# Optimization experiments

Hardware: AMD Instinct MI355X
Metric: run time of the kernel (lower is better)

The kernel has to match this reference:

```python
import jax, jax.numpy as jnp
import numpy as np

N_HEAD = 16
LN_EPS = 1e-5     # torch LayerNorm default
ATTN_EPS = 1e-6   # fast-transformers CausalLinearAttention eps


def layer_norm(x, g, b):
    mu = x.mean(-1, keepdims=True)
    var = ((x - mu) ** 2).mean(-1, keepdims=True)
    return (x - mu) * jax.lax.rsqrt(var + LN_EPS) * g + b


def favor(x, omega):
    # Favor/Performer softmax-kernel features.
    # x: [B,S,H,dh], omega: [dh, m/2] -> phi: [B,S,H,m] with m = 2*(dh//2) = dh
    dh = x.shape[-1]
    m = 2 * omega.shape[-1]
    xs = x * (dh ** -0.25)  # x * sqrt(softmax_temp), softmax_temp = 1/sqrt(dh)
    u = jnp.einsum('bshd,dm->bshm', xs, omega)
    h = 0.5 * jnp.sum(xs * xs, axis=-1, keepdims=True)  # ||x||^2 / 2
    return jnp.concatenate([jnp.exp(u - h), jnp.exp(-u - h)], axis=-1) * (m ** -0.5)


def causal_linear_attention(q, k, v):
    # q,k: [B,S,H,M] feature-mapped; v: [B,S,H,Dv]
    # out[i] = (phiQ_i @ sum_{j<=i} phiK_j v_j^T) / (phiQ_i . sum_{j<=i} phiK_j)
    B, S, H, M = q.shape
    Dv = v.shape[-1]
    qT = jnp.moveaxis(q, 1, 0)  # [S,B,H,M]
    kT = jnp.moveaxis(k, 1, 0)
    vT = jnp.moveaxis(v, 1, 0)  # [S,B,H,Dv]
    S0 = jnp.zeros((B, H, M, Dv), q.dtype)
    z0 = jnp.zeros((B, H, M), q.dtype)

    def step(carry, qkv):
        Sst, zst = carry
        qi, ki, vi = qkv
        Sst = Sst + ki[..., :, None] * vi[..., None, :]  # [B,H,M,Dv]
        zst = zst + ki                                   # [B,H,M]
        num = jnp.einsum('bhm,bhmd->bhd', qi, Sst)
        den = jnp.einsum('bhm,bhm->bh', qi, zst) + ATTN_EPS
        return (Sst, zst), num / den[..., None]

    _, out = jax.lax.scan(step, (S0, z0), (qT, kT, vT))
    return jnp.moveaxis(out, 0, 1)  # [B,S,H,Dv]


def forward(x, Wq, bq, Wk, bk, Wv, bv, Wo, bo, omega,
            ln1_g, ln1_b, ln2_g, ln2_b, W1, bf1, W2, bf2):
    L = Wq.shape[0]
    B, S, D = x.shape
    dh = D // N_HEAD
    out = x
    for l in range(L):  # fixed small layer count
        q = (out @ Wq[l] + bq[l]).reshape(B, S, N_HEAD, dh)
        k = (out @ Wk[l] + bk[l]).reshape(B, S, N_HEAD, dh)
        v = (out @ Wv[l] + bv[l]).reshape(B, S, N_HEAD, dh)
        Qf = favor(q, omega[l])
        Kf = favor(k, omega[l])
        a = causal_linear_attention(Qf, Kf, v).reshape(B, S, D)
        a = a @ Wo[l] + bo[l]
        h = layer_norm(out + a, ln1_g[l], ln1_b[l])          # norm1 (post-norm)
        y = jax.nn.relu(h @ W1[l] + bf1[l]) @ W2[l] + bf2[l]  # FFN
        out = layer_norm(h + y, ln2_g[l], ln2_b[l])          # norm2
    return out


def setup_inputs() -> dict:
    key = jax.random.key(0)
    L, B, S, D, DFF = 3, 2, 1024, 1024, 4096
    dh = D // N_HEAD
    ks = jax.random.split(key, 8)
    g = lambda k, shape: jax.random.normal(k, shape, jnp.float32) * 0.02
    return {
        'x': jax.random.normal(ks[0], (B, S, D), jnp.float32),
        'Wq': g(ks[1], (L, D, D)), 'bq': jnp.zeros((L, D), jnp.float32),
        'Wk': g(ks[2], (L, D, D)), 'bk': jnp.zeros((L, D), jnp.float32),
        'Wv': g(ks[3], (L, D, D)), 'bv': jnp.zeros((L, D), jnp.float32),
        'Wo': g(ks[4], (L, D, D)), 'bo': jnp.zeros((L, D), jnp.float32),
        'omega': jax.random.normal(ks[5], (L, dh, dh // 2), jnp.float32),
        'ln1_g': jnp.ones((L, D), jnp.float32), 'ln1_b': jnp.zeros((L, D), jnp.float32),
        'ln2_g': jnp.ones((L, D), jnp.float32), 'ln2_b': jnp.zeros((L, D), jnp.float32),
        'W1': g(ks[6], (L, D, DFF)), 'bf1': jnp.zeros((L, DFF), jnp.float32),
        'W2': g(ks[7], (L, DFF, D)), 'bf2': jnp.zeros((L, D), jnp.float32),
    }


def reference(x, Wq, bq, Wk, bk, Wv, bv, Wo, bo, omega,
              ln1_g, ln1_b, ln2_g, ln2_b, W1, bf1, W2, bf2):
    return forward(x, Wq, bq, Wk, bk, Wv, bv, Wo, bo, omega,
                   ln1_g, ln1_b, ln2_g, ln2_b, W1, bf1, W2, bf2)
```

## Files before the change

### kernel.cpp

```cpp
#include <hip/hip_runtime.h>

typedef unsigned int u32;
typedef unsigned short u16;
typedef unsigned long long u64;

#define LN_EPS 1e-5f
#define ATTN_EPS 1e-6f

typedef __bf16 bf16x8 __attribute__((ext_vector_type(8)));
typedef short shortx8 __attribute__((ext_vector_type(8)));
typedef float fx4 __attribute__((ext_vector_type(4)));
typedef float fx16 __attribute__((ext_vector_type(16)));

__device__ __forceinline__ u16 f2bf(float f){
  union{float f; u32 u;} x; x.f = f;
  u32 r = 0x7fffu + ((x.u>>16)&1u);
  return (u16)((x.u + r)>>16);
}
__device__ __forceinline__ float bf2f(u16 u){
  union{u32 u; float f;} x; x.u = ((u32)u)<<16; return x.f;
}
__device__ __forceinline__ bf16x8 ldfrag(const u16* p){
  return __builtin_bit_cast(bf16x8, *(const shortx8*)p);
}

__device__ __forceinline__ void async16(const void* g, void* l){
  typedef const __attribute__((address_space(1))) void gas_t;
  typedef __attribute__((address_space(3))) void las_t;
  __builtin_amdgcn_global_load_lds((gas_t*)(u64)g, (las_t*)(u32)(u64)l, 16, 0, 0);
}

__global__ void detect_kernel(const u16* __restrict__ ln1g, int* __restrict__ flag){
  if (threadIdx.x == 0 && blockIdx.x == 0)
    *flag = (ln1g[0] == 0x3F80u) ? 1 : 0;
}

__global__ __launch_bounds__(256) void cvt_small(
    const void* p0, const void* p1, const void* p2, const void* p3,
    const void* p4, const void* p5, const void* p6, const void* p7,
    const void* p8, const void* p9, const void* p10,
    float* __restrict__ out, const int* __restrict__ flagp)
{
  int i = blockIdx.x*256 + threadIdx.x;
  if (i >= 46080) return;
  const void* src; int off;
  if      (i < 3072)  { src=p0;  off=i; }
  else if (i < 6144)  { src=p1;  off=i-3072; }
  else if (i < 9216)  { src=p2;  off=i-6144; }
  else if (i < 12288) { src=p3;  off=i-9216; }
  else if (i < 18432) { src=p4;  off=i-12288; }
  else if (i < 21504) { src=p5;  off=i-18432; }
  else if (i < 24576) { src=p6;  off=i-21504; }
  else if (i < 27648) { src=p7;  off=i-24576; }
  else if (i < 30720) { src=p8;  off=i-27648; }
  else if (i < 43008) { src=p9;  off=i-30720; }
  else                { src=p10; off=i-43008; }
  float v;
  if (*flagp){ union{u32 u; float f;} x; x.u = ((u32)((const u16*)src)[off])<<16; v = x.f; }
  else v = ((const float*)src)[off];
  out[i] = v;
}

__global__ __launch_bounds__(256) void cvt_x(const void* __restrict__ in, float* __restrict__ out,
                                             u16* __restrict__ outbf, int n, const int* __restrict__ flagp){
  int i = blockIdx.x*256 + threadIdx.x;
  if (i >= n) return;
  float v;
  if (*flagp){ union{u32 u; float f;} x; x.u = ((u32)((const u16*)in)[i])<<16; v = x.f; }
  else v = ((const float*)in)[i];
  out[i] = v;
  outbf[i] = f2bf(v);
}

__global__ __launch_bounds__(256) void transpose_cvtL(
    const void* __restrict__ W, u16* __restrict__ Wt,
    int K, int N, size_t zsrc, size_t zdst, const int* __restrict__ flagp)
{
  __shared__ float s[32][33];
  const size_t eoff = (size_t)blockIdx.z * zsrc;
  Wt += (size_t)blockIdx.z * zdst;
  const int bx = blockIdx.x, by = blockIdx.y;
  const int tid = threadIdx.x;
  const int c = tid & 31, r = tid >> 5;
  const int isbf = *flagp;
#pragma unroll
  for (int i = 0; i < 4; ++i){
    int k = by*32 + r + i*8, n = bx*32 + c;
    size_t idx = eoff + (size_t)k*N + n;
    float v;
    if (isbf){ union{u32 u; float f;} x; x.u = ((u32)((const u16*)W)[idx])<<16; v = x.f; }
    else v = ((const float*)W)[idx];
    s[r + i*8][c] = v;
  }
  __syncthreads();
#pragma unroll
  for (int i = 0; i < 4; ++i){
    int n = bx*32 + r + i*8, k = by*32 + c;
    Wt[(size_t)n*K + k] = f2bf(s[c][r + i*8]);
  }
}

__global__ __launch_bounds__(256) void transpose_cvtQ(
    const void* __restrict__ W0, const void* __restrict__ W1,
    const void* __restrict__ W2, const void* __restrict__ W3,
    u16* __restrict__ Wt, const int* __restrict__ flagp)
{
  __shared__ float s[32][33];
  const int z = blockIdx.z, l = z >> 2, m = z & 3;
  const void* W = (m==0)?W0:((m==1)?W1:((m==2)?W2:W3));
  const size_t eoff = (size_t)l * 1048576;
  Wt += (size_t)z * 1048576;
  const int bx = blockIdx.x, by = blockIdx.y;
  const int tid = threadIdx.x;
  const int c = tid & 31, r = tid >> 5;
  const int isbf = *flagp;
#pragma unroll
  for (int i = 0; i < 4; ++i){
    int k = by*32 + r + i*8, n = bx*32 + c;
    size_t idx = eoff + (size_t)k*1024 + n;
    float v;
    if (isbf){ union{u32 u; float f;} x; x.u = ((u32)((const u16*)W)[idx])<<16; v = x.f; }
    else v = ((const float*)W)[idx];
    s[r + i*8][c] = v;
  }
  __syncthreads();
#pragma unroll
  for (int i = 0; i < 4; ++i){
    int n = bx*32 + r + i*8, k = by*32 + c;
    Wt[(size_t)n*1024 + k] = f2bf(s[c][r + i*8]);
  }
}

__global__ __launch_bounds__(512, 2) void mfma_gemm8(
    const u16* __restrict__ A, const u16* __restrict__ W,
    const float* __restrict__ bias,
    float* __restrict__ C, u16* __restrict__ Cbf,
    int N, int Kst, int kstep_z, int klen,
    size_t wz, size_t cz, int bz, int bias_all, int relu)
{
  __shared__ u16 As[3][256*64];
  __shared__ u16 Bs[3][128*64];
  const int z = blockIdx.z;
  W    += (size_t)z * wz;
  bias += (size_t)z * bz;
  if (C) C += (size_t)z * cz;
  const int kbeg = z * kstep_z;
  const int tid = threadIdx.x;
  const int lane = tid & 63, wid = tid >> 6;
  const size_t KstS = (size_t)Kst;

  int bx = blockIdx.x, by = blockIdx.y;
  {
    const int gx = gridDim.x, gy = gridDim.y;
    if (((gx & 3) == 0) && ((gy & 1) == 0)) {
      const int cw = gx >> 2, ch = gy >> 1;
      if (((cw & (cw-1)) == 0) && ((ch & (ch-1)) == 0)) {
        const int o = by*gx + bx;
        const int xcd = o & 7, k = o >> 3;
        const int lgw = 31 - __clz(cw);
        bx = (xcd & 3)*cw + (k & (cw-1));
        by = (xcd >> 2)*ch + (k >> lgw);
      }
    }
  }
  const int row0 = by * 256, col0 = bx * 128;

  const int sR = tid >> 3;
  const int sC = ((tid & 7) ^ (sR & 7)) << 3;
  const u16* gAr = A + (size_t)(row0 + sR)*KstS + kbeg + sC;
  const u16* gBr = W + (size_t)(col0 + sR)*KstS + kbeg + sC;

#define STAGE_H0(b, ks) { const size_t ko = (size_t)(ks) << 6; \
    async16(gAr + ko,                &As[b][tid*8]); \
    async16(gAr + 64*KstS + ko,      &As[b][4096 + tid*8]); \
    async16(gBr + ko,                &Bs[b][tid*8]); }
#define STAGE_H1(b, ks) { const size_t ko = (size_t)(ks) << 6; \
    async16(gAr + 128*KstS + ko,     &As[b][8192 + tid*8]); \
    async16(gAr + 192*KstS + ko,     &As[b][12288 + tid*8]); \
    async16(gBr + 64*KstS + ko,      &Bs[b][4096 + tid*8]); }

  const int nt = klen >> 6;
  STAGE_H0(0, 0) STAGE_H1(0, 0)
  STAGE_H0(1, 1) STAGE_H1(1, 1)
  __builtin_amdgcn_s_waitcnt(0x0F76);
  __builtin_amdgcn_s_barrier();

  const int l31 = lane & 31, hi = lane >> 5;
  const int wr = (wid >> 1) * 64;
  const int wc = (wid & 1) * 64;
  fx16 acc[2][2] = {};

  for (int t = 0; t < nt; ++t){
    const int buf = t % 3;
    const int nx   = (t + 2 < nt) ? (t + 2) : (nt - 1);
    const int nbuf = (t + 2) % 3;

    bf16x8 a0[2][2], b0[2][2];
#pragma unroll
    for (int kk = 0; kk < 2; ++kk){
      const int sl = ((2*kk + hi) ^ (l31 & 7)) << 3;
#pragma unroll
      for (int mt = 0; mt < 2; ++mt)
        a0[mt][kk] = ldfrag(&As[buf][(wr + mt*32 + l31)*64 + sl]);
#pragma unroll
      for (int ntc = 0; ntc < 2; ++ntc)
        b0[ntc][kk] = ldfrag(&Bs[buf][(wc + ntc*32 + l31)*64 + sl]);
    }
    STAGE_H0(nbuf, nx)
    __builtin_amdgcn_s_barrier();
    __builtin_amdgcn_s_setprio(1);
#pragma unroll
    for (int kk = 0; kk < 2; ++kk)
#pragma unroll
      for (int mt = 0; mt < 2; ++mt)
#pragma unroll
        for (int ntc = 0; ntc < 2; ++ntc)
          acc[mt][ntc] = __builtin_amdgcn_mfma_f32_32x32x16_bf16(a0[mt][kk], b0[ntc][kk], acc[mt][ntc], 0,0,0);
    __builtin_amdgcn_s_setprio(0);
    __builtin_amdgcn_s_barrier();

    bf16x8 a1[2][2], b1[2][2];
#pragma unroll
    for (int kk = 0; kk < 2; ++kk){
      const int sl = ((2*(kk+2) + hi) ^ (l31 & 7)) << 3;
#pragma unroll
      for (int mt = 0; mt < 2; ++mt)
        a1[mt][kk] = ldfrag(&As[buf][(wr + mt*32 + l31)*64 + sl]);
#pragma unroll
      for (int ntc = 0; ntc < 2; ++ntc)
        b1[ntc][kk] = ldfrag(&Bs[buf][(wc + ntc*32 + l31)*64 + sl]);
    }
    STAGE_H1(nbuf, nx)
    __builtin_amdgcn_s_waitcnt(0x0F76);
    __builtin_amdgcn_s_barrier();
    __builtin_amdgcn_s_setprio(1);
#pragma unroll
    for (int kk = 0; kk < 2; ++kk)
#pragma unroll
      for (int mt = 0; mt < 2; ++mt)
#pragma unroll
        for (int ntc = 0; ntc < 2; ++ntc)
          acc[mt][ntc] = __builtin_amdgcn_mfma_f32_32x32x16_bf16(a1[mt][kk], b1[ntc][kk], acc[mt][ntc], 0,0,0);
    __builtin_amdgcn_s_setprio(0);
    __builtin_amdgcn_s_barrier();
  }
  __builtin_amdgcn_s_waitcnt(0x0F70);

  const int rbase = 4*hi;
#pragma unroll
  for (int ntc = 0; ntc < 2; ++ntc){
    const int col = col0 + wc + ntc*32 + l31;
    const float bv = (bias_all || z == 0) ? bias[col] : 0.f;
#pragma unroll
    for (int mt = 0; mt < 2; ++mt){
#pragma unroll
      for (int r = 0; r < 16; ++r){
        const int row = row0 + wr + mt*32 + rbase + (r & 3) + 8*(r >> 2);
        float v = acc[mt][ntc][r] + bv;
        if (relu) v = fmaxf(v, 0.f);
        if (C)   C[(size_t)row*N + col] = v;
        if (Cbf) Cbf[(size_t)row*N + col] = f2bf(v);
      }
    }
  }
#undef STAGE_H0
#undef STAGE_H1
}

__global__ __launch_bounds__(256) void favor_kernel(
    float* __restrict__ Q, float* __restrict__ Kp, const float* __restrict__ omega,
    u16* __restrict__ Qb, u16* __restrict__ Kb)
{
  __shared__ float sh[4][64];
  __shared__ float sho[64][32];
  int tid = threadIdx.x;
  for (int i = tid; i < 2048; i += 256)
    sho[i>>5][i&31] = omega[i];
  int wv = tid >> 6, lane = tid & 63;
  int th = blockIdx.x*4 + wv;
  size_t base = (size_t)(th >> 4) * 1024 + (size_t)(th & 15) * 64;
  int jm = lane & 31;
  float sgn = (lane < 32) ? 1.f : -1.f;
  for (int w = 0; w < 2; ++w){
    float* p = w ? Kp : Q;
    float xs = p[base + lane] * 0.35355339059327373f;
    __syncthreads();
    sh[wv][lane] = xs;
    __syncthreads();
    float u = 0.f, hh = 0.f;
#pragma unroll
    for (int d = 0; d < 64; ++d){
      float xv = sh[wv][d];
      u  = fmaf(xv, sho[d][jm], u);
      hh = fmaf(xv, xv, hh);
    }
    float phi = expf(sgn*u - 0.5f*hh) * 0.125f;
    if (w) p[base + lane] = phi;
    (w ? Kb : Qb)[base + lane] = f2bf(phi);
  }
}

__global__ __launch_bounds__(256) void chunk_kv(
    const float* __restrict__ Kf, const float* __restrict__ V,
    float* __restrict__ KV, float* __restrict__ Ksum)
{
  __shared__ float Ks[64][64];
  __shared__ float Vs[64][64];
  int blk = blockIdx.x;
  int c = blk & 15, h = (blk >> 4) & 15, b = blk >> 8;
  int tid = threadIdx.x;
  for (int i = tid; i < 1024; i += 256){
    int j = i >> 4, m4 = (i & 15) << 2;
    size_t src = ((size_t)(b*1024 + c*64 + j)*16 + h)*64 + m4;
    *(float4*)&Ks[j][m4] = *(const float4*)&Kf[src];
    *(float4*)&Vs[j][m4] = *(const float4*)&V[src];
  }
  __syncthreads();
  int m = tid & 63, dg = tid >> 6;
  float acc[16] = {0.f};
  for (int j = 0; j < 64; ++j){
    float kv = Ks[j][m];
#pragma unroll
    for (int di = 0; di < 16; ++di)
      acc[di] = fmaf(Vs[j][dg*16+di], kv, acc[di]);
  }
  size_t outb = (size_t)blk * 4096;
#pragma unroll
  for (int di = 0; di < 16; ++di)
    KV[outb + (size_t)(dg*16+di)*64 + m] = acc[di];
  if (tid < 64){
    float s = 0.f;
    for (int j = 0; j < 64; ++j) s += Ks[j][tid];
    Ksum[(size_t)blk*64 + tid] = s;
  }
}

__global__ __launch_bounds__(256) void chunk_scan(float* __restrict__ KV, float* __restrict__ Ksum)
{
  int blk = blockIdx.x;
  int bh = blk >> 4, ec = blk & 15;
  int e = ec*256 + threadIdx.x;
  size_t base = (size_t)bh * 65536 + e;
  float run = 0.f;
  for (int c = 0; c < 16; ++c){
    size_t idx = base + (size_t)c*4096;
    float t = KV[idx]; KV[idx] = run; run += t;
  }
  if (ec == 0 && threadIdx.x < 64){
    size_t kb = (size_t)bh * 1024 + threadIdx.x;
    float rz = 0.f;
    for (int c = 0; c < 16; ++c){
      size_t idx = kb + c*64;
      float t = Ksum[idx]; Ksum[idx] = rz; rz += t;
    }
  }
}

__global__ __launch_bounds__(256) void attn_kernel(
    const u16* __restrict__ Qbf, const u16* __restrict__ Kbf,
    const float* __restrict__ V, const float* __restrict__ KVt,
    const float* __restrict__ Ksum, u16* __restrict__ Outbf)
{
  __shared__ u16 Qs[64][72];
  __shared__ u16 Ks[64][72];
  __shared__ u16 Ss[64][72];
  __shared__ u16 Vt[64][72];
  __shared__ u16 Pt[64][72];
  __shared__ float Vrow[64][68];
  __shared__ float densum[64];

  const int blk = blockIdx.x;
  const int c = blk & 15, h = (blk >> 4) & 15, b = blk >> 8;
  const int tid = threadIdx.x;
  const int lane = tid & 63, w = tid >> 6;
  const int quad = lane >> 4, l16 = lane & 15;
  const int t0 = b*1024 + c*64;

  {
    const int r = tid >> 2, q4 = (tid & 3) << 4;
    size_t g = (size_t)(t0 + r)*1024 + h*64 + q4;
    *(uint4*)&Qs[r][q4]   = *(const uint4*)(Qbf + g);
    *(uint4*)&Qs[r][q4+8] = *(const uint4*)(Qbf + g + 8);
    *(uint4*)&Ks[r][q4]   = *(const uint4*)(Kbf + g);
    *(uint4*)&Ks[r][q4+8] = *(const uint4*)(Kbf + g + 8);
    const float* vg = V + g;
    *(float4*)&Vrow[r][q4+0]  = *(const float4*)(vg+0);
    *(float4*)&Vrow[r][q4+4]  = *(const float4*)(vg+4);
    *(float4*)&Vrow[r][q4+8]  = *(const float4*)(vg+8);
    *(float4*)&Vrow[r][q4+12] = *(const float4*)(vg+12);
    const float* pg = KVt + (size_t)blk*4096 + r*64 + q4;
    u16 tmp[16];
#pragma unroll
    for (int j = 0; j < 16; ++j) tmp[j] = f2bf(pg[j]);
    *(uint4*)&Pt[r][q4]   = *(uint4*)&tmp[0];
    *(uint4*)&Pt[r][q4+8] = *(uint4*)&tmp[8];
  }
  __syncthreads();
  {
    const int d = tid >> 2, j16 = (tid & 3) << 4;
    u16 tmp[16];
#pragma unroll
    for (int j = 0; j < 16; ++j) tmp[j] = f2bf(Vrow[j16+j][d]);
    *(uint4*)&Vt[d][j16]   = *(uint4*)&tmp[0];
    *(uint4*)&Vt[d][j16+8] = *(uint4*)&tmp[8];
  }

  const int iw0 = w*16;
  bf16x8 aq0 = ldfrag(&Qs[iw0+l16][quad*8]);
  bf16x8 aq1 = ldfrag(&Qs[iw0+l16][32+quad*8]);
  fx4 sacc[4];
#pragma unroll
  for (int u = 0; u < 4; ++u){
    sacc[u] = (fx4){0.f,0.f,0.f,0.f};
    bf16x8 b0 = ldfrag(&Ks[u*16+l16][quad*8]);
    bf16x8 b1 = ldfrag(&Ks[u*16+l16][32+quad*8]);
    sacc[u] = __builtin_amdgcn_mfma_f32_16x16x32_bf16(aq0, b0, sacc[u], 0, 0, 0);
    sacc[u] = __builtin_amdgcn_mfma_f32_16x16x32_bf16(aq1, b1, sacc[u], 0, 0, 0);
  }
  float rs[4] = {0.f,0.f,0.f,0.f};
#pragma unroll
  for (int u = 0; u < 4; ++u){
    const int jl = u*16 + l16;
#pragma unroll
    for (int r = 0; r < 4; ++r){
      const int il = iw0 + quad*4 + r;
      float v = (jl <= il) ? sacc[u][r] : 0.f;
      rs[r] += v;
      Ss[il][jl] = f2bf(v);
    }
  }
#pragma unroll
  for (int off = 1; off < 16; off <<= 1){
#pragma unroll
    for (int r = 0; r < 4; ++r) rs[r] += __shfl_xor(rs[r], off);
  }
  if (l16 == 0){
#pragma unroll
    for (int r = 0; r < 4; ++r) densum[iw0 + quad*4 + r] = rs[r];
  }
  __syncthreads();

  {
    const int row = iw0 + l16;
    const float* zp = Ksum + (size_t)blk*64;
    float dp = 0.f;
#pragma unroll
    for (int m = 0; m < 16; ++m){
      const int mm = quad*16 + m;
      dp = fmaf(bf2f(Qs[row][mm]), zp[mm], dp);
    }
    dp += __shfl_xor(dp, 16);
    dp += __shfl_xor(dp, 32);
    if (quad == 0) densum[row] = densum[row] + dp + ATTN_EPS;
  }
  __syncthreads();

  bf16x8 as0 = ldfrag(&Ss[iw0+l16][quad*8]);
  bf16x8 as1 = ldfrag(&Ss[iw0+l16][32+quad*8]);
  fx4 oacc[4];
#pragma unroll
  for (int u = 0; u < 4; ++u){
    const int d0 = u*16;
    oacc[u] = (fx4){0.f,0.f,0.f,0.f};
    oacc[u] = __builtin_amdgcn_mfma_f32_16x16x32_bf16(as0, ldfrag(&Vt[d0+l16][quad*8]),    oacc[u], 0,0,0);
    oacc[u] = __builtin_amdgcn_mfma_f32_16x16x32_bf16(as1, ldfrag(&Vt[d0+l16][32+quad*8]), oacc[u], 0,0,0);
    oacc[u] = __builtin_amdgcn_mfma_f32_16x16x32_bf16(aq0, ldfrag(&Pt[d0+l16][quad*8]),    oacc[u], 0,0,0);
    oacc[u] = __builtin_amdgcn_mfma_f32_16x16x32_bf16(aq1, ldfrag(&Pt[d0+l16][32+quad*8]), oacc[u], 0,0,0);
  }
#pragma unroll
  for (int u = 0; u < 4; ++u){
    const int d = u*16 + l16;
#pragma unroll
    for (int r = 0; r < 4; ++r){
      const int il = iw0 + quad*4 + r;
      const float o = oacc[u][r] / densum[il];
      Outbf[(size_t)(t0 + il)*1024 + h*64 + d] = f2bf(o);
    }
  }
}

__global__ __launch_bounds__(256) void resid_ln(
    const float* __restrict__ X, const float* __restrict__ Y0, const float* __restrict__ Y1,
    const float* __restrict__ Y2, const float* __restrict__ Y3,
    const float* __restrict__ g, const float* __restrict__ b,
    float* __restrict__ Dst, u16* __restrict__ DstBf,
    void* __restrict__ OutPtr, const int* __restrict__ flagp)
{
  __shared__ float rs[4], rss[4];
  int row = blockIdx.x, tid = threadIdx.x;
  int lane = tid & 63, wv = tid >> 6;
  size_t base = (size_t)row * 1024;
  int c = tid << 2;
  float4 xv = *(const float4*)&X[base + c];
  float4 y0 = *(const float4*)&Y0[base + c];
  float4 y1 = *(const float4*)&Y1[base + c];
  float v0 = xv.x+y0.x+y1.x, v1 = xv.y+y0.y+y1.y, v2 = xv.z+y0.z+y1.z, v3 = xv.w+y0.w+y1.w;
  if (Y2){
    float4 y2 = *(const float4*)&Y2[base + c];
    float4 y3 = *(const float4*)&Y3[base + c];
    v0 += y2.x + y3.x; v1 += y2.y + y3.y; v2 += y2.z + y3.z; v3 += y2.w + y3.w;
  }
  float s = v0+v1+v2+v3;
  float ss = v0*v0+v1*v1+v2*v2+v3*v3;
  for (int off = 32; off; off >>= 1){
    s  += __shfl_down(s, off);
    ss += __shfl_down(ss, off);
  }
  if (lane == 0){ rs[wv] = s; rss[wv] = ss; }
  __syncthreads();
  float S  = rs[0]+rs[1]+rs[2]+rs[3];
  float SS = rss[0]+rss[1]+rss[2]+rss[3];
  float mu = S * (1.f/1024.f);
  float var = SS * (1.f/1024.f) - mu*mu;
  float rinv = rsqrtf(var + LN_EPS);
  float4 gv = *(const float4*)(g + c);
  float4 bb = *(const float4*)(b + c);
  float o0 = (v0-mu)*rinv*gv.x + bb.x;
  float o1 = (v1-mu)*rinv*gv.y + bb.y;
  float o2 = (v2-mu)*rinv*gv.z + bb.z;
  float o3 = (v3-mu)*rinv*gv.w + bb.w;
  *(float4*)&Dst[base + c] = make_float4(o0,o1,o2,o3);
  uint2 ob;
  ob.x = (u32)f2bf(o0) | ((u32)f2bf(o1) << 16);
  ob.y = (u32)f2bf(o2) | ((u32)f2bf(o3) << 16);
  *(uint2*)(DstBf + base + c) = ob;
  if (OutPtr){
    if (*flagp){
      *(uint2*)((u16*)OutPtr + base + c) = ob;
    } else {
      *(float4*)((float*)OutPtr + base + c) = make_float4(o0,o1,o2,o3);
    }
  }
}

extern "C" void kernel_launch(void* const* d_in, const int* in_sizes, int n_in,
                              void* d_out, int out_size, void* d_ws, size_t ws_size,
                              hipStream_t stream)
{
  (void)in_sizes; (void)n_in; (void)out_size; (void)ws_size;

  float* ws   = (float*)d_ws;
  float* R    = ws;
  float* P0   = R  + 2097152;
  float* P1   = P0 + 2097152;
  float* P2   = P1 + 2097152;
  float* P3   = P2 + 2097152;
  float* KVb  = P3 + 2097152;
  float* Ks   = KVb + 2097152;
  float* smallP = Ks + 32768;
  float* pend = smallP + 46080;
  int* flag = (int*)pend;
  u16* abf  = (u16*)(pend + 4);
  u16* hbf  = abf  + 2097152;
  u16* t1bf = hbf  + 2097152;
  u16* fbf  = t1bf + 2097152;
  u16* qpbf = fbf  + 8388608;
  u16* kpbf = qpbf + 2097152;
  u16* WtQ  = kpbf + 2097152;
  u16* WtF1 = WtQ  + 12582912;
  u16* WtF2 = WtF1 + 12582912;

  float* bqF  = smallP + 0;
  float* boF  = smallP + 9216;
  float* omF  = smallP + 12288;
  float* l1gF = smallP + 18432;
  float* l1bF = smallP + 21504;
  float* l2gF = smallP + 24576;
  float* l2bF = smallP + 27648;
  float* bf1F = smallP + 30720;
  float* bf2F = smallP + 43008;

  detect_kernel<<<1, 64, 0, stream>>>((const u16*)d_in[10], flag);
  cvt_small<<<180, 256, 0, stream>>>(d_in[2], d_in[4], d_in[6], d_in[8], d_in[9],
                                     d_in[10], d_in[11], d_in[12], d_in[13],
                                     d_in[15], d_in[17], smallP, flag);
  cvt_x<<<8192, 256, 0, stream>>>(d_in[0], R, abf, 2097152, flag);

  transpose_cvtQ<<<dim3(32, 32, 12), 256, 0, stream>>>(d_in[1], d_in[3], d_in[5], d_in[7],
                                                       WtQ, flag);
  transpose_cvtL<<<dim3(128, 32, 3), 256, 0, stream>>>(d_in[14], WtF1, 1024, 4096,
                                                       4194304, 4194304, flag);
  transpose_cvtL<<<dim3(32, 128, 3), 256, 0, stream>>>(d_in[16], WtF2, 4096, 1024,
                                                       4194304, 4194304, flag);

  dim3 gQKV(8, 8, 3);
  dim3 gO(8, 8, 2);
  dim3 gF1(32, 8, 1);
  dim3 gF2(8, 8, 4);

  for (int l = 0; l < 3; ++l){
    const size_t wQ = (size_t)l * 4194304;

    mfma_gemm8<<<gQKV, 512, 0, stream>>>(abf, WtQ + wQ, bqF + l*1024, P0, (u16*)nullptr,
                                         1024, 1024, 0, 1024,
                                         1048576, 2097152, 3072, 1, 0);
    favor_kernel<<<8192, 256, 0, stream>>>(P0, P1, omF + l*2048, qpbf, kpbf);
    chunk_kv<<<512, 256, 0, stream>>>(P1, P2, KVb, Ks);
    chunk_scan<<<512, 256, 0, stream>>>(KVb, Ks);
    attn_kernel<<<512, 256, 0, stream>>>(qpbf, kpbf, P2, KVb, Ks, t1bf);

    mfma_gemm8<<<gO, 512, 0, stream>>>(t1bf, WtQ + wQ + 3145728, boF + l*1024, P0, (u16*)nullptr,
                                       1024, 1024, 512, 512,
                                       0, 2097152, 0, 0, 0);
    resid_ln<<<2048, 256, 0, stream>>>(R, P0, P1, nullptr, nullptr,
                                       l1gF + l*1024, l1bF + l*1024,
                                       KVb, hbf, nullptr, flag);

    mfma_gemm8<<<gF1, 512, 0, stream>>>(hbf, WtF1 + wQ, bf1F + l*4096, (float*)nullptr, fbf,
                                        4096, 1024, 0, 1024,
                                        0, 0, 0, 1, 1);

    mfma_gemm8<<<gF2, 512, 0, stream>>>(fbf, WtF2 + wQ, bf2F + l*1024, P0, (u16*)nullptr,
                                        1024, 4096, 1024, 1024,
                                        0, 2097152, 0, 0, 0);

    resid_ln<<<2048, 256, 0, stream>>>(KVb, P0, P1, P2, P3,
                                       l2gF + l*1024, l2bF + l*1024,
                                       R, abf, (l == 2) ? d_out : nullptr, flag);
  }
}
```

Baseline: 721.3 us.

## Fuse FAVOR feature map into chunk_kv and attention kernels

```diff
diff --git a/kernel.cpp b/kernel.cpp
--- a/kernel.cpp
+++ b/kernel.cpp
@@ -267,59 +267,70 @@
 #undef STAGE_H1
 }
 
-__global__ __launch_bounds__(256) void favor_kernel(
-    float* __restrict__ Q, float* __restrict__ Kp, const float* __restrict__ omega,
-    u16* __restrict__ Qb, u16* __restrict__ Kb)
-{
-  __shared__ float sh[4][64];
-  __shared__ float sho[64][32];
-  int tid = threadIdx.x;
+__global__ __launch_bounds__(256) void chunk_kv_favor(
+    const float* __restrict__ Kraw, const float* __restrict__ V,
+    const float* __restrict__ omega,
+    float* __restrict__ KV, float* __restrict__ Ksum, u16* __restrict__ Kb)
+{
+  __shared__ float Xs[64][68];
+  __shared__ float Vs[64][64];
+  __shared__ float Ph[64][68];
+  __shared__ float Om[64][32];
+  const int blk = blockIdx.x;
+  const int c = blk & 15, h = (blk >> 4) & 15, b = blk >> 8;
+  const int tid = threadIdx.x;
+  const int t0 = b*1024 + c*64;
+
   for (int i = tid; i < 2048; i += 256)
-    sho[i>>5][i&31] = omega[i];
-  int wv = tid >> 6, lane = tid & 63;
-  int th = blockIdx.x*4 + wv;
-  size_t base = (size_t)(th >> 4) * 1024 + (size_t)(th & 15) * 64;
-  int jm = lane & 31;
-  float sgn = (lane < 32) ? 1.f : -1.f;
-  for (int w = 0; w < 2; ++w){
-    float* p = w ? Kp : Q;
-    float xs = p[base + lane] * 0.35355339059327373f;
-    __syncthreads();
-    sh[wv][lane] = xs;
-    __syncthreads();
-    float u = 0.f, hh = 0.f;
-#pragma unroll
-    for (int d = 0; d < 64; ++d){
-      float xv = sh[wv][d];
-      u  = fmaf(xv, sho[d][jm], u);
-      hh = fmaf(xv, xv, hh);
-    }
-    float phi = expf(sgn*u - 0.5f*hh) * 0.125f;
-    if (w) p[base + lane] = phi;
-    (w ? Kb : Qb)[base + lane] = f2bf(phi);
-  }
-}
-
-__global__ __launch_bounds__(256) void chunk_kv(
-    const float* __restrict__ Kf, const float* __restrict__ V,
-    float* __restrict__ KV, float* __restrict__ Ksum)
-{
-  __shared__ float Ks[64][64];
-  __shared__ float Vs[64][64];
-  int blk = blockIdx.x;
-  int c = blk & 15, h = (blk >> 4) & 15, b = blk >> 8;
-  int tid = threadIdx.x;
+    Om[i>>5][i&31] = omega[i];
   for (int i = tid; i < 1024; i += 256){
     int j = i >> 4, m4 = (i & 15) << 2;
-    size_t src = ((size_t)(b*1024 + c*64 + j)*16 + h)*64 + m4;
-    *(float4*)&Ks[j][m4] = *(const float4*)&Kf[src];
+    size_t src = (size_t)(t0 + j)*1024 + h*64 + m4;
+    float4 kv4 = *(const float4*)&Kraw[src];
+    float4 xs4 = make_float4(kv4.x*0.35355339059327373f, kv4.y*0.35355339059327373f,
+                             kv4.z*0.35355339059327373f, kv4.w*0.35355339059327373f);
+    *(float4*)&Xs[j][m4] = xs4;
     *(float4*)&Vs[j][m4] = *(const float4*)&V[src];
   }
   __syncthreads();
-  int m = tid & 63, dg = tid >> 6;
+
+  {
+    const int tok = tid >> 2, q = tid & 3;
+    float u[8] = {0,0,0,0,0,0,0,0};
+    float hh = 0.f;
+    for (int d = 0; d < 64; ++d){
+      float xv = Xs[tok][d];
+      hh = fmaf(xv, xv, hh);
+      float4 o0 = *(const float4*)&Om[d][q*8];
+      float4 o1 = *(const float4*)&Om[d][q*8+4];
+      u[0]=fmaf(xv,o0.x,u[0]); u[1]=fmaf(xv,o0.y,u[1]);
+      u[2]=fmaf(xv,o0.z,u[2]); u[3]=fmaf(xv,o0.w,u[3]);
+      u[4]=fmaf(xv,o1.x,u[4]); u[5]=fmaf(xv,o1.y,u[5]);
+      u[6]=fmaf(xv,o1.z,u[6]); u[7]=fmaf(xv,o1.w,u[7]);
+    }
+    hh *= 0.5f;
+#pragma unroll
+    for (int i = 0; i < 8; ++i){
+      Ph[tok][q*8+i]    = expf( u[i] - hh) * 0.125f;
+      Ph[tok][32+q*8+i] = expf(-u[i] - hh) * 0.125f;
+    }
+  }
+  __syncthreads();
+
+  {
+    const int r = tid >> 2, c4 = (tid & 3) << 4;
+    u16 tmp[16];
+#pragma unroll
+    for (int j = 0; j < 16; ++j) tmp[j] = f2bf(Ph[r][c4 + j]);
+    size_t g = (size_t)(t0 + r)*1024 + h*64 + c4;
+    *(uint4*)(Kb + g)     = *(uint4*)&tmp[0];
+    *(uint4*)(Kb + g + 8) = *(uint4*)&tmp[8];
+  }
+
+  const int m = tid & 63, dg = tid >> 6;
   float acc[16] = {0.f};
   for (int j = 0; j < 64; ++j){
-    float kv = Ks[j][m];
+    float kv = Ph[j][m];
 #pragma unroll
     for (int di = 0; di < 16; ++di)
       acc[di] = fmaf(Vs[j][dg*16+di], kv, acc[di]);
@@ -330,7 +341,7 @@
     KV[outb + (size_t)(dg*16+di)*64 + m] = acc[di];
   if (tid < 64){
     float s = 0.f;
-    for (int j = 0; j < 64; ++j) s += Ks[j][tid];
+    for (int j = 0; j < 64; ++j) s += Ph[j][tid];
     Ksum[(size_t)blk*64 + tid] = s;
   }
 }
@@ -357,9 +368,10 @@
 }
 
 __global__ __launch_bounds__(256) void attn_kernel(
-    const u16* __restrict__ Qbf, const u16* __restrict__ Kbf,
+    const float* __restrict__ Qraw, const u16* __restrict__ Kbf,
     const float* __restrict__ V, const float* __restrict__ KVt,
-    const float* __restrict__ Ksum, u16* __restrict__ Outbf)
+    const float* __restrict__ Ksum, const float* __restrict__ omega,
+    u16* __restrict__ Outbf)
 {
   __shared__ u16 Qs[64][72];
   __shared__ u16 Ks[64][72];
@@ -367,6 +379,7 @@
   __shared__ u16 Vt[64][72];
   __shared__ u16 Pt[64][72];
   __shared__ float Vrow[64][68];
+  __shared__ float Om[64][32];
   __shared__ float densum[64];
 
   const int blk = blockIdx.x;
@@ -375,12 +388,12 @@
   const int lane = tid & 63, w = tid >> 6;
   const int quad = lane >> 4, l16 = lane & 15;
   const int t0 = b*1024 + c*64;
-
-  {
-    const int r = tid >> 2, q4 = (tid & 3) << 4;
-    size_t g = (size_t)(t0 + r)*1024 + h*64 + q4;
-    *(uint4*)&Qs[r][q4]   = *(const uint4*)(Qbf + g);
-    *(uint4*)&Qs[r][q4+8] = *(const uint4*)(Qbf + g + 8);
+  const int r = tid >> 2, q4 = (tid & 3) << 4;
+  const size_t g = (size_t)(t0 + r)*1024 + h*64 + q4;
+
+  for (int i = tid; i < 2048; i += 256)
+    Om[i>>5][i&31] = omega[i];
+  {
     *(uint4*)&Ks[r][q4]   = *(const uint4*)(Kbf + g);
     *(uint4*)&Ks[r][q4+8] = *(const uint4*)(Kbf + g + 8);
     const float* vg = V + g;
@@ -404,6 +417,44 @@
     *(uint4*)&Vt[d][j16]   = *(uint4*)&tmp[0];
     *(uint4*)&Vt[d][j16+8] = *(uint4*)&tmp[8];
   }
+  __syncthreads();
+  {
+    const float* qg = Qraw + g;
+    float4 a0 = *(const float4*)(qg+0), a1 = *(const float4*)(qg+4);
+    float4 a2 = *(const float4*)(qg+8), a3 = *(const float4*)(qg+12);
+    const float sc = 0.35355339059327373f;
+    *(float4*)&Vrow[r][q4+0]  = make_float4(a0.x*sc, a0.y*sc, a0.z*sc, a0.w*sc);
+    *(float4*)&Vrow[r][q4+4]  = make_float4(a1.x*sc, a1.y*sc, a1.z*sc, a1.w*sc);
+    *(float4*)&Vrow[r][q4+8]  = make_float4(a2.x*sc, a2.y*sc, a2.z*sc, a2.w*sc);
+    *(float4*)&Vrow[r][q4+12] = make_float4(a3.x*sc, a3.y*sc, a3.z*sc, a3.w*sc);
+  }
+  __syncthreads();
+  {
+    const int tok = tid >> 2, q = tid & 3;
+    float u[8] = {0,0,0,0,0,0,0,0};
+    float hh = 0.f;
+    for (int d = 0; d < 64; ++d){
+      float xv = Vrow[tok][d];
+      hh = fmaf(xv, xv, hh);
+      float4 o0 = *(const float4*)&Om[d][q*8];
+      float4 o1 = *(const float4*)&Om[d][q*8+4];
+      u[0]=fmaf(xv,o0.x,u[0]); u[1]=fmaf(xv,o0.y,u[1]);
+      u[2]=fmaf(xv,o0.z,u[2]); u[3]=fmaf(xv,o0.w,u[3]);
+      u[4]=fmaf(xv,o1.x,u[4]); u[5]=fmaf(xv,o1.y,u[5]);
+      u[6]=fmaf(xv,o1.z,u[6]); u[7]=fmaf(xv,o1.w,u[7]);
+    }
+    hh *= 0.5f;
+#pragma unroll
+    for (int i = 0; i < 8; i += 2){
+      float e0 = expf( u[i]   - hh) * 0.125f;
+      float e1 = expf( u[i+1] - hh) * 0.125f;
+      *(u32*)&Qs[tok][q*8+i]    = (u32)f2bf(e0) | ((u32)f2bf(e1) << 16);
+      float f0 = expf(-u[i]   - hh) * 0.125f;
+      float f1 = expf(-u[i+1] - hh) * 0.125f;
+      *(u32*)&Qs[tok][32+q*8+i] = (u32)f2bf(f0) | ((u32)f2bf(f1) << 16);
+    }
+  }
+  __syncthreads();
 
   const int iw0 = w*16;
   bf16x8 aq0 = ldfrag(&Qs[iw0+l16][quad*8]);
@@ -422,21 +473,21 @@
   for (int u = 0; u < 4; ++u){
     const int jl = u*16 + l16;
 #pragma unroll
-    for (int r = 0; r < 4; ++r){
-      const int il = iw0 + quad*4 + r;
-      float v = (jl <= il) ? sacc[u][r] : 0.f;
-      rs[r] += v;
+    for (int rr = 0; rr < 4; ++rr){
+      const int il = iw0 + quad*4 + rr;
+      float v = (jl <= il) ? sacc[u][rr] : 0.f;
+      rs[rr] += v;
       Ss[il][jl] = f2bf(v);
     }
   }
 #pragma unroll
   for (int off = 1; off < 16; off <<= 1){
 #pragma unroll
-    for (int r = 0; r < 4; ++r) rs[r] += __shfl_xor(rs[r], off);
+    for (int rr = 0; rr < 4; ++rr) rs[rr] += __shfl_xor(rs[rr], off);
   }
   if (l16 == 0){
 #pragma unroll
-    for (int r = 0; r < 4; ++r) densum[iw0 + quad*4 + r] = rs[r];
+    for (int rr = 0; rr < 4; ++rr) densum[iw0 + quad*4 + rr] = rs[rr];
   }
   __syncthreads();
 
@@ -471,9 +522,9 @@
   for (int u = 0; u < 4; ++u){
     const int d = u*16 + l16;
 #pragma unroll
-    for (int r = 0; r < 4; ++r){
-      const int il = iw0 + quad*4 + r;
-      const float o = oacc[u][r] / densum[il];
+    for (int rr = 0; rr < 4; ++rr){
+      const int il = iw0 + quad*4 + rr;
+      const float o = oacc[u][rr] / densum[il];
       Outbf[(size_t)(t0 + il)*1024 + h*64 + d] = f2bf(o);
     }
   }
@@ -554,8 +605,7 @@
   u16* hbf  = abf  + 2097152;
   u16* t1bf = hbf  + 2097152;
   u16* fbf  = t1bf + 2097152;
-  u16* qpbf = fbf  + 8388608;
-  u16* kpbf = qpbf + 2097152;
+  u16* kpbf = fbf  + 8388608;
   u16* WtQ  = kpbf + 2097152;
   u16* WtF1 = WtQ  + 12582912;
   u16* WtF2 = WtF1 + 12582912;
@@ -594,10 +644,9 @@
     mfma_gemm8<<<gQKV, 512, 0, stream>>>(abf, WtQ + wQ, bqF + l*1024, P0, (u16*)nullptr,
                                          1024, 1024, 0, 1024,
                                          1048576, 2097152, 3072, 1, 0);
-    favor_kernel<<<8192, 256, 0, stream>>>(P0, P1, omF + l*2048, qpbf, kpbf);
-    chunk_kv<<<512, 256, 0, stream>>>(P1, P2, KVb, Ks);
+    chunk_kv_favor<<<512, 256, 0, stream>>>(P1, P2, omF + l*2048, KVb, Ks, kpbf);
     chunk_scan<<<512, 256, 0, stream>>>(KVb, Ks);
-    attn_kernel<<<512, 256, 0, stream>>>(qpbf, kpbf, P2, KVb, Ks, t1bf);
+    attn_kernel<<<512, 256, 0, stream>>>(P0, kpbf, P2, KVb, Ks, omF + l*2048, t1bf);
 
     mfma_gemm8<<<gO, 512, 0, stream>>>(t1bf, WtQ + wQ + 3145728, boF + l*1024, P0, (u16*)nullptr,
                                        1024, 1024, 512, 512,
```

New measurement: 678.7 us. 5.9% less time.
